# Optimization experiments

Hardware: AMD Instinct MI355X
Metric: run time of the kernel (lower is better)

Reference implementation:

```python
import jax, jax.numpy as jnp
import numpy as np

E, H, BLOCK = 1024, 64, 2048

def setup_inputs() -> dict:
    key = jax.random.key(0)
    kx, kk, kq, kv = jax.random.split(key, 4)
    s = 1.0 / np.sqrt(E)
    return {
        "x": jax.random.normal(kx, (16, 2048, E), dtype=jnp.float32),
        "Wk": jax.random.uniform(kk, (E, H), jnp.float32, -s, s),
        "Wq": jax.random.uniform(kq, (E, H), jnp.float32, -s, s),
        "Wv": jax.random.uniform(kv, (E, H), jnp.float32, -s, s),
    }

def reference(x, Wk, Wq, Wv):
    B, T, C = x.shape
    k = x @ Wk  # [B,T,H]
    q = x @ Wq
    v = x @ Wv
    scale = jnp.asarray(H, x.dtype) ** -0.5
    wei = jnp.einsum("bth,bsh->bts", q, k) * scale  # [B,T,T]
    causal = jnp.tril(jnp.ones((T, T), dtype=bool))
    wei = jnp.where(causal, wei, -jnp.inf)
    wei = jax.nn.softmax(wei, axis=-1)
    # dropout is identity in eval mode
    return jnp.einsum("bts,bsh->bth", wei, v)
```

## Files before the change

### kernel.cpp

```cpp
#include <hip/hip_runtime.h>


typedef __bf16 bf16x8 __attribute__((ext_vector_type(8)));
typedef float f32x4 __attribute__((ext_vector_type(4)));

constexpr int kE = 1024;
constexpr int kH = 64;
constexpr int kT = 2048;
constexpr int kB = 16;
constexpr int kM = kB * kT;
constexpr float kQScale = 0.125f * 1.44269504088896340736f;

#define MFMA16(a, b, c) __builtin_amdgcn_mfma_f32_16x16x32_bf16((a), (b), (c), 0, 0, 0)

__global__ __launch_bounds__(256)
void prep_w(const float* __restrict__ Wq, const float* __restrict__ Wk,
            const float* __restrict__ Wv, __bf16* __restrict__ WbT)
{
    __shared__ float tl[64][65];
    const int mat = blockIdx.x >> 4;
    const int k0 = (blockIdx.x & 15) * 64;
    const float* src = (mat == 0) ? Wq : (mat == 1) ? Wk : Wv;

    const int t = threadIdx.x;
    const int kr = t >> 2;
    const int cg = (t & 3) * 16;
    #pragma unroll
    for (int i = 0; i < 4; ++i) {
        float4 v = *(const float4*)&src[(size_t)(k0 + kr) * kH + cg + 4 * i];
        tl[cg + 4 * i + 0][kr] = v.x;
        tl[cg + 4 * i + 1][kr] = v.y;
        tl[cg + 4 * i + 2][kr] = v.z;
        tl[cg + 4 * i + 3][kr] = v.w;
    }
    __syncthreads();
    const int nl = t >> 2;
    const int kg = (t & 3) * 16;
    bf16x8 o0, o1;
    #pragma unroll
    for (int j = 0; j < 8; ++j) {
        o0[j] = (__bf16)tl[nl][kg + j];
        o1[j] = (__bf16)tl[nl][kg + 8 + j];
    }
    *(bf16x8*)&WbT[(size_t)(mat * 64 + nl) * kE + k0 + kg] = o0;
    *(bf16x8*)&WbT[(size_t)(mat * 64 + nl) * kE + k0 + kg + 8] = o1;
}

__global__ __launch_bounds__(256)
void qkv(const float* __restrict__ x, const __bf16* __restrict__ WbT,
         __bf16* __restrict__ qo, __bf16* __restrict__ ko, __bf16* __restrict__ vo)
{
    __shared__ __align__(16) __bf16 As[64][72];
    __shared__ __align__(16) __bf16 Bs[192][72];

    const int t = threadIdx.x;
    const int lane = t & 63;
    const int w = t >> 6;
    const int l15 = lane & 15;
    const int q = lane >> 4;
    const int row0 = blockIdx.x * 64;

    f32x4 acc[4][3];
    #pragma unroll
    for (int mt = 0; mt < 4; ++mt)
        #pragma unroll
        for (int nt = 0; nt < 3; ++nt) acc[mt][nt] = (f32x4){0.f, 0.f, 0.f, 0.f};

    const int sm = t >> 2;
    const int sc = (t & 3) * 16;

    for (int k0 = 0; k0 < kE; k0 += 64) {
        {
            float4 v0 = *(const float4*)&x[(size_t)(row0 + sm) * kE + k0 + sc];
            float4 v1 = *(const float4*)&x[(size_t)(row0 + sm) * kE + k0 + sc + 4];
            float4 v2 = *(const float4*)&x[(size_t)(row0 + sm) * kE + k0 + sc + 8];
            float4 v3 = *(const float4*)&x[(size_t)(row0 + sm) * kE + k0 + sc + 12];
            bf16x8 b0, b1;
            b0[0] = (__bf16)v0.x; b0[1] = (__bf16)v0.y; b0[2] = (__bf16)v0.z; b0[3] = (__bf16)v0.w;
            b0[4] = (__bf16)v1.x; b0[5] = (__bf16)v1.y; b0[6] = (__bf16)v1.z; b0[7] = (__bf16)v1.w;
            b1[0] = (__bf16)v2.x; b1[1] = (__bf16)v2.y; b1[2] = (__bf16)v2.z; b1[3] = (__bf16)v2.w;
            b1[4] = (__bf16)v3.x; b1[5] = (__bf16)v3.y; b1[6] = (__bf16)v3.z; b1[7] = (__bf16)v3.w;
            *(bf16x8*)&As[sm][sc] = b0;
            *(bf16x8*)&As[sm][sc + 8] = b1;
        }
        #pragma unroll
        for (int j = 0; j < 6; ++j) {
            int id = t + 256 * j;
            int n = id >> 3;
            int kc = (id & 7) * 8;
            *(bf16x8*)&Bs[n][kc] = *(const bf16x8*)&WbT[(size_t)n * kE + k0 + kc];
        }
        __syncthreads();

        #pragma unroll
        for (int ks = 0; ks < 2; ++ks) {
            bf16x8 a4[4];
            #pragma unroll
            for (int mt = 0; mt < 4; ++mt)
                a4[mt] = *(const bf16x8*)&As[mt * 16 + l15][ks * 32 + q * 8];
            #pragma unroll
            for (int nt = 0; nt < 3; ++nt) {
                bf16x8 b = *(const bf16x8*)&Bs[w * 48 + nt * 16 + l15][ks * 32 + q * 8];
                #pragma unroll
                for (int mt = 0; mt < 4; ++mt)
                    acc[mt][nt] = MFMA16(a4[mt], b, acc[mt][nt]);
            }
        }
        __syncthreads();
    }

    #pragma unroll
    for (int nt = 0; nt < 3; ++nt) {
        const int col0 = w * 48 + nt * 16;
        const int mat = col0 >> 6;
        const int c = (col0 & 63) + l15;
        __bf16* dst = (mat == 0) ? qo : (mat == 1) ? ko : vo;
        const float sc_ = (mat == 0) ? kQScale : 1.0f;
        #pragma unroll
        for (int mt = 0; mt < 4; ++mt)
            #pragma unroll
            for (int r = 0; r < 4; ++r) {
                const size_t row = row0 + mt * 16 + q * 4 + r;
                dst[row * kH + c] = (__bf16)(acc[mt][nt][r] * sc_);
            }
    }
}

__global__ __launch_bounds__(256)
void attn(const __bf16* __restrict__ qm, const __bf16* __restrict__ km,
          const __bf16* __restrict__ vm, float* __restrict__ out)
{
    __shared__ __align__(16) __bf16 Qs[64][72];
    __shared__ __align__(16) __bf16 Ks[64][72];
    __shared__ __align__(16) __bf16 Vt[64][72];
    __shared__ __align__(16) __bf16 Ps[4][16][72];

    const int t = threadIdx.x;
    const int lane = t & 63;
    const int w = t >> 6;
    const int l15 = lane & 15;
    const int q = lane >> 4;

    const int batch = blockIdx.x & 15;
    const int qi = 31 - (blockIdx.x >> 4);
    const int q0 = qi * 64;

    const __bf16* qb = qm + (size_t)batch * kT * kH;
    const __bf16* kb = km + (size_t)batch * kT * kH;
    const __bf16* vb = vm + (size_t)batch * kT * kH;

    const int sm = t >> 2;
    const int sc = (t & 3) * 16;

    *(bf16x8*)&Qs[sm][sc]     = *(const bf16x8*)&qb[(size_t)(q0 + sm) * kH + sc];
    *(bf16x8*)&Qs[sm][sc + 8] = *(const bf16x8*)&qb[(size_t)(q0 + sm) * kH + sc + 8];
    bf16x8 aq[2];
    #pragma unroll
    for (int ks = 0; ks < 2; ++ks)
        aq[ks] = *(const bf16x8*)&Qs[w * 16 + l15][ks * 32 + q * 8];

    f32x4 O[4];
    float m4[4], l4[4];
    #pragma unroll
    for (int i = 0; i < 4; ++i) {
        O[i] = (f32x4){0.f, 0.f, 0.f, 0.f};
        m4[i] = -1e30f; l4[i] = 0.f;
    }

    for (int kt = 0; kt <= qi; ++kt) {
        const int s0 = kt * 64;
        *(bf16x8*)&Ks[sm][sc]     = *(const bf16x8*)&kb[(size_t)(s0 + sm) * kH + sc];
        *(bf16x8*)&Ks[sm][sc + 8] = *(const bf16x8*)&kb[(size_t)(s0 + sm) * kH + sc + 8];
        {
            bf16x8 v0 = *(const bf16x8*)&vb[(size_t)(s0 + sm) * kH + sc];
            bf16x8 v1 = *(const bf16x8*)&vb[(size_t)(s0 + sm) * kH + sc + 8];
            #pragma unroll
            for (int j = 0; j < 8; ++j) {
                Vt[sc + j][sm] = v0[j];
                Vt[sc + 8 + j][sm] = v1[j];
            }
        }
        __syncthreads();

        f32x4 sacc[4];
        #pragma unroll
        for (int nt = 0; nt < 4; ++nt) sacc[nt] = (f32x4){0.f, 0.f, 0.f, 0.f};
        #pragma unroll
        for (int ks = 0; ks < 2; ++ks)
            #pragma unroll
            for (int nt = 0; nt < 4; ++nt) {
                bf16x8 b = *(const bf16x8*)&Ks[nt * 16 + l15][ks * 32 + q * 8];
                sacc[nt] = MFMA16(aq[ks], b, sacc[nt]);
            }

        if (kt == qi) {
            #pragma unroll
            for (int nt = 0; nt < 4; ++nt) {
                const int scol = s0 + nt * 16 + l15;
                #pragma unroll
                for (int r = 0; r < 4; ++r)
                    if (scol > q0 + w * 16 + q * 4 + r) sacc[nt][r] = -1e30f;
            }
        }

        #pragma unroll
        for (int r = 0; r < 4; ++r) {
            float mx = fmaxf(fmaxf(sacc[0][r], sacc[1][r]), fmaxf(sacc[2][r], sacc[3][r]));
            #pragma unroll
            for (int off = 1; off < 16; off <<= 1)
                mx = fmaxf(mx, __shfl_xor(mx, off, 16));
            const float mnew = fmaxf(m4[r], mx);
            const float alpha = __builtin_amdgcn_exp2f(m4[r] - mnew);
            float rs = 0.f;
            #pragma unroll
            for (int nt = 0; nt < 4; ++nt) {
                const float p = __builtin_amdgcn_exp2f(sacc[nt][r] - mnew);
                sacc[nt][r] = p;
                rs += p;
            }
            #pragma unroll
            for (int off = 1; off < 16; off <<= 1)
                rs += __shfl_xor(rs, off, 16);
            l4[r] = l4[r] * alpha + rs;
            m4[r] = mnew;
            #pragma unroll
            for (int ht = 0; ht < 4; ++ht) O[ht][r] *= alpha;
            #pragma unroll
            for (int nt = 0; nt < 4; ++nt)
                Ps[w][q * 4 + r][nt * 16 + l15] = (__bf16)sacc[nt][r];
        }

        #pragma unroll
        for (int ss = 0; ss < 2; ++ss) {
            bf16x8 ap = *(const bf16x8*)&Ps[w][l15][ss * 32 + q * 8];
            #pragma unroll
            for (int ht = 0; ht < 4; ++ht) {
                bf16x8 bv = *(const bf16x8*)&Vt[ht * 16 + l15][ss * 32 + q * 8];
                O[ht] = MFMA16(ap, bv, O[ht]);
            }
        }
        __syncthreads();
    }

    #pragma unroll
    for (int r = 0; r < 4; ++r) {
        const float inv = 1.0f / l4[r];
        const size_t row = (size_t)batch * kT + q0 + w * 16 + q * 4 + r;
        #pragma unroll
        for (int ht = 0; ht < 4; ++ht)
            out[row * kH + ht * 16 + l15] = O[ht][r] * inv;
    }
}

extern "C" void kernel_launch(void* const* d_in, const int* in_sizes, int n_in,
                              void* d_out, int out_size, void* d_ws, size_t ws_size,
                              hipStream_t stream)
{
    (void)in_sizes; (void)n_in; (void)out_size; (void)ws_size;
    const float* x  = (const float*)d_in[0];
    const float* Wk = (const float*)d_in[1];
    const float* Wq = (const float*)d_in[2];
    const float* Wv = (const float*)d_in[3];

    __bf16* WbT = (__bf16*)d_ws;
    __bf16* qb = WbT + (size_t)192 * kE;
    __bf16* kbuf = qb + (size_t)kM * kH;
    __bf16* vbuf = kbuf + (size_t)kM * kH;

    prep_w<<<48, 256, 0, stream>>>(Wq, Wk, Wv, WbT);
    qkv<<<kM / 64, 256, 0, stream>>>(x, WbT, qb, kbuf, vbuf);
    attn<<<kB * (kT / 64), 256, 0, stream>>>(qb, kbuf, vbuf, (float*)d_out);
}
```

Measured before the change: 271.6 us.

## Write V transposed in projection and restructure attention to single-wave register-fed blocks

The projection kernel now writes V transposed per batch ([B,H,T]) so the attention kernel can load V fragments straight from global memory without an LDS transpose. Attention is recast as one 64-thread wave per 16-query tile, with the MFMA operands swapped so S is computed transposed. K fragments are double-buffered in registers and prefetched from global, which removes the shared K/V tiles and block-wide barriers. The cost is more global/L2 traffic, since K/V tiles are no longer shared across four waves, plus a grid four times larger with smaller blocks.

```diff
diff --git a/kernel.cpp b/kernel.cpp
--- a/kernel.cpp
+++ b/kernel.cpp
@@ -2,6 +2,7 @@
 
 
 typedef __bf16 bf16x8 __attribute__((ext_vector_type(8)));
+typedef __bf16 bf16x4 __attribute__((ext_vector_type(4)));
 typedef float f32x4 __attribute__((ext_vector_type(4)));
 
 constexpr int kE = 1024;
@@ -48,7 +49,7 @@
 
 __global__ __launch_bounds__(256)
 void qkv(const float* __restrict__ x, const __bf16* __restrict__ WbT,
-         __bf16* __restrict__ qo, __bf16* __restrict__ ko, __bf16* __restrict__ vo)
+         __bf16* __restrict__ qo, __bf16* __restrict__ ko, __bf16* __restrict__ vT)
 {
     __shared__ __align__(16) __bf16 As[64][72];
     __shared__ __align__(16) __bf16 Bs[192][72];
@@ -109,78 +110,88 @@
         __syncthreads();
     }
 
+    const int batch = row0 >> 11;
+    const int tr0 = row0 & 2047;
     #pragma unroll
     for (int nt = 0; nt < 3; ++nt) {
         const int col0 = w * 48 + nt * 16;
         const int mat = col0 >> 6;
         const int c = (col0 & 63) + l15;
-        __bf16* dst = (mat == 0) ? qo : (mat == 1) ? ko : vo;
-        const float sc_ = (mat == 0) ? kQScale : 1.0f;
-        #pragma unroll
-        for (int mt = 0; mt < 4; ++mt)
-            #pragma unroll
-            for (int r = 0; r < 4; ++r) {
-                const size_t row = row0 + mt * 16 + q * 4 + r;
-                dst[row * kH + c] = (__bf16)(acc[mt][nt][r] * sc_);
+        if (mat == 2) {
+            #pragma unroll
+            for (int mt = 0; mt < 4; ++mt) {
+                const int trow = tr0 + mt * 16 + q * 4;
+                bf16x4 pk;
+                #pragma unroll
+                for (int r = 0; r < 4; ++r) pk[r] = (__bf16)acc[mt][nt][r];
+                *(bf16x4*)&vT[((size_t)batch * kH + c) * kT + trow] = pk;
             }
-    }
-}
-
-__global__ __launch_bounds__(256)
+        } else {
+            __bf16* dst = (mat == 0) ? qo : ko;
+            const float sc_ = (mat == 0) ? kQScale : 1.0f;
+            #pragma unroll
+            for (int mt = 0; mt < 4; ++mt)
+                #pragma unroll
+                for (int r = 0; r < 4; ++r) {
+                    const size_t row = row0 + mt * 16 + q * 4 + r;
+                    dst[row * kH + c] = (__bf16)(acc[mt][nt][r] * sc_);
+                }
+        }
+    }
+}
+
+__device__ __forceinline__ void load_kfrag(bf16x8 kf[8], const __bf16* kb,
+                                           int s0, int l15, int Q)
+{
+    #pragma unroll
+    for (int ks = 0; ks < 2; ++ks)
+        #pragma unroll
+        for (int nt = 0; nt < 4; ++nt)
+            kf[ks * 4 + nt] =
+                *(const bf16x8*)&kb[(size_t)(s0 + nt * 16 + l15) * kH + ks * 32 + Q * 8];
+}
+
+__global__ __launch_bounds__(64)
 void attn(const __bf16* __restrict__ qm, const __bf16* __restrict__ km,
-          const __bf16* __restrict__ vm, float* __restrict__ out)
-{
-    __shared__ __align__(16) __bf16 Qs[64][72];
-    __shared__ __align__(16) __bf16 Ks[64][72];
-    __shared__ __align__(16) __bf16 Vt[64][72];
-    __shared__ __align__(16) __bf16 Ps[4][16][72];
-
-    const int t = threadIdx.x;
-    const int lane = t & 63;
-    const int w = t >> 6;
+          const __bf16* __restrict__ vT, float* __restrict__ out)
+{
+    __shared__ __align__(16) __bf16 Ps[16][72];
+
+    const int lane = threadIdx.x;
     const int l15 = lane & 15;
-    const int q = lane >> 4;
+    const int Q = lane >> 4;
 
     const int batch = blockIdx.x & 15;
-    const int qi = 31 - (blockIdx.x >> 4);
-    const int q0 = qi * 64;
+    const int q16 = 127 - (blockIdx.x >> 4);
+    const int qrow = q16 * 16 + l15;
+    const int last = q16 >> 2;
 
     const __bf16* qb = qm + (size_t)batch * kT * kH;
     const __bf16* kb = km + (size_t)batch * kT * kH;
-    const __bf16* vb = vm + (size_t)batch * kT * kH;
-
-    const int sm = t >> 2;
-    const int sc = (t & 3) * 16;
-
-    *(bf16x8*)&Qs[sm][sc]     = *(const bf16x8*)&qb[(size_t)(q0 + sm) * kH + sc];
-    *(bf16x8*)&Qs[sm][sc + 8] = *(const bf16x8*)&qb[(size_t)(q0 + sm) * kH + sc + 8];
+    const __bf16* vb = vT + (size_t)batch * kH * kT;
+
     bf16x8 aq[2];
-    #pragma unroll
-    for (int ks = 0; ks < 2; ++ks)
-        aq[ks] = *(const bf16x8*)&Qs[w * 16 + l15][ks * 32 + q * 8];
+    aq[0] = *(const bf16x8*)&qb[(size_t)qrow * kH + Q * 8];
+    aq[1] = *(const bf16x8*)&qb[(size_t)qrow * kH + 32 + Q * 8];
 
     f32x4 O[4];
-    float m4[4], l4[4];
-    #pragma unroll
-    for (int i = 0; i < 4; ++i) {
-        O[i] = (f32x4){0.f, 0.f, 0.f, 0.f};
-        m4[i] = -1e30f; l4[i] = 0.f;
-    }
-
-    for (int kt = 0; kt <= qi; ++kt) {
+    #pragma unroll
+    for (int i = 0; i < 4; ++i) O[i] = (f32x4){0.f, 0.f, 0.f, 0.f};
+    float m_ = -3.0e38f, l_ = 0.f;
+
+    bf16x8 kfa[8], kfb[8];
+    load_kfrag(kfa, kb, 0, l15, Q);
+
+    auto step = [&](bf16x8 (&kcur)[8], bf16x8 (&knxt)[8], int kt) {
         const int s0 = kt * 64;
-        *(bf16x8*)&Ks[sm][sc]     = *(const bf16x8*)&kb[(size_t)(s0 + sm) * kH + sc];
-        *(bf16x8*)&Ks[sm][sc + 8] = *(const bf16x8*)&kb[(size_t)(s0 + sm) * kH + sc + 8];
-        {
-            bf16x8 v0 = *(const bf16x8*)&vb[(size_t)(s0 + sm) * kH + sc];
-            bf16x8 v1 = *(const bf16x8*)&vb[(size_t)(s0 + sm) * kH + sc + 8];
-            #pragma unroll
-            for (int j = 0; j < 8; ++j) {
-                Vt[sc + j][sm] = v0[j];
-                Vt[sc + 8 + j][sm] = v1[j];
-            }
-        }
-        __syncthreads();
+        bf16x8 vf[8];
+        #pragma unroll
+        for (int ht = 0; ht < 4; ++ht)
+            #pragma unroll
+            for (int ss = 0; ss < 2; ++ss)
+                vf[ht * 2 + ss] =
+                    *(const bf16x8*)&vb[(size_t)(ht * 16 + l15) * kT + s0 + ss * 32 + Q * 8];
+        if (kt < last) load_kfrag(knxt, kb, s0 + 64, l15, Q);
 
         f32x4 sacc[4];
         #pragma unroll
@@ -188,67 +199,72 @@
         #pragma unroll
         for (int ks = 0; ks < 2; ++ks)
             #pragma unroll
-            for (int nt = 0; nt < 4; ++nt) {
-                bf16x8 b = *(const bf16x8*)&Ks[nt * 16 + l15][ks * 32 + q * 8];
-                sacc[nt] = MFMA16(aq[ks], b, sacc[nt]);
-            }
-
-        if (kt == qi) {
-            #pragma unroll
-            for (int nt = 0; nt < 4; ++nt) {
-                const int scol = s0 + nt * 16 + l15;
+            for (int nt = 0; nt < 4; ++nt)
+                sacc[nt] = MFMA16(kcur[ks * 4 + nt], aq[ks], sacc[nt]);
+
+        if (kt == last) {
+            #pragma unroll
+            for (int nt = 0; nt < 4; ++nt)
                 #pragma unroll
                 for (int r = 0; r < 4; ++r)
-                    if (scol > q0 + w * 16 + q * 4 + r) sacc[nt][r] = -1e30f;
-            }
-        }
-
-        #pragma unroll
-        for (int r = 0; r < 4; ++r) {
-            float mx = fmaxf(fmaxf(sacc[0][r], sacc[1][r]), fmaxf(sacc[2][r], sacc[3][r]));
-            #pragma unroll
-            for (int off = 1; off < 16; off <<= 1)
-                mx = fmaxf(mx, __shfl_xor(mx, off, 16));
-            const float mnew = fmaxf(m4[r], mx);
-            const float alpha = __builtin_amdgcn_exp2f(m4[r] - mnew);
-            float rs = 0.f;
-            #pragma unroll
-            for (int nt = 0; nt < 4; ++nt) {
+                    if (s0 + nt * 16 + Q * 4 + r > qrow) sacc[nt][r] = -3.0e38f;
+        }
+
+        float mx = sacc[0][0];
+        #pragma unroll
+        for (int nt = 0; nt < 4; ++nt)
+            #pragma unroll
+            for (int r = 0; r < 4; ++r) mx = fmaxf(mx, sacc[nt][r]);
+        mx = fmaxf(mx, __shfl_xor(mx, 16));
+        mx = fmaxf(mx, __shfl_xor(mx, 32));
+        const float mnew = fmaxf(m_, mx);
+        const float alpha = __builtin_amdgcn_exp2f(m_ - mnew);
+        float rs = 0.f;
+        #pragma unroll
+        for (int nt = 0; nt < 4; ++nt)
+            #pragma unroll
+            for (int r = 0; r < 4; ++r) {
                 const float p = __builtin_amdgcn_exp2f(sacc[nt][r] - mnew);
                 sacc[nt][r] = p;
                 rs += p;
             }
-            #pragma unroll
-            for (int off = 1; off < 16; off <<= 1)
-                rs += __shfl_xor(rs, off, 16);
-            l4[r] = l4[r] * alpha + rs;
-            m4[r] = mnew;
-            #pragma unroll
-            for (int ht = 0; ht < 4; ++ht) O[ht][r] *= alpha;
-            #pragma unroll
-            for (int nt = 0; nt < 4; ++nt)
-                Ps[w][q * 4 + r][nt * 16 + l15] = (__bf16)sacc[nt][r];
-        }
-
-        #pragma unroll
-        for (int ss = 0; ss < 2; ++ss) {
-            bf16x8 ap = *(const bf16x8*)&Ps[w][l15][ss * 32 + q * 8];
-            #pragma unroll
-            for (int ht = 0; ht < 4; ++ht) {
-                bf16x8 bv = *(const bf16x8*)&Vt[ht * 16 + l15][ss * 32 + q * 8];
-                O[ht] = MFMA16(ap, bv, O[ht]);
-            }
-        }
-        __syncthreads();
-    }
-
-    #pragma unroll
-    for (int r = 0; r < 4; ++r) {
-        const float inv = 1.0f / l4[r];
-        const size_t row = (size_t)batch * kT + q0 + w * 16 + q * 4 + r;
-        #pragma unroll
-        for (int ht = 0; ht < 4; ++ht)
-            out[row * kH + ht * 16 + l15] = O[ht][r] * inv;
+        rs += __shfl_xor(rs, 16);
+        rs += __shfl_xor(rs, 32);
+        l_ = l_ * alpha + rs;
+        m_ = mnew;
+        #pragma unroll
+        for (int ht = 0; ht < 4; ++ht) O[ht] *= alpha;
+
+        #pragma unroll
+        for (int nt = 0; nt < 4; ++nt) {
+            bf16x4 pk;
+            #pragma unroll
+            for (int r = 0; r < 4; ++r) pk[r] = (__bf16)sacc[nt][r];
+            *(bf16x4*)&Ps[l15][nt * 16 + Q * 4] = pk;
+        }
+        bf16x8 pb0 = *(const bf16x8*)&Ps[l15][Q * 8];
+        bf16x8 pb1 = *(const bf16x8*)&Ps[l15][32 + Q * 8];
+
+        #pragma unroll
+        for (int ht = 0; ht < 4; ++ht) {
+            O[ht] = MFMA16(vf[ht * 2 + 0], pb0, O[ht]);
+            O[ht] = MFMA16(vf[ht * 2 + 1], pb1, O[ht]);
+        }
+    };
+
+    for (int kt = 0; kt <= last; kt += 2) {
+        step(kfa, kfb, kt);
+        if (kt + 1 <= last) step(kfb, kfa, kt + 1);
+    }
+
+    const float inv = 1.0f / l_;
+    float* orow = out + ((size_t)batch * kT + qrow) * kH;
+    #pragma unroll
+    for (int ht = 0; ht < 4; ++ht) {
+        float4 o4;
+        o4.x = O[ht][0] * inv; o4.y = O[ht][1] * inv;
+        o4.z = O[ht][2] * inv; o4.w = O[ht][3] * inv;
+        *(float4*)&orow[ht * 16 + Q * 4] = o4;
     }
 }
 
@@ -263,11 +279,11 @@
     const float* Wv = (const float*)d_in[3];
 
     __bf16* WbT = (__bf16*)d_ws;
-    __bf16* qb = WbT + (size_t)192 * kE;
+    __bf16* qb  = WbT + (size_t)192 * kE;
     __bf16* kbuf = qb + (size_t)kM * kH;
-    __bf16* vbuf = kbuf + (size_t)kM * kH;
+    __bf16* vT   = kbuf + (size_t)kM * kH;
 
     prep_w<<<48, 256, 0, stream>>>(Wq, Wk, Wv, WbT);
-    qkv<<<kM / 64, 256, 0, stream>>>(x, WbT, qb, kbuf, vbuf);
-    attn<<<kB * (kT / 64), 256, 0, stream>>>(qb, kbuf, vbuf, (float*)d_out);
-}
+    qkv<<<kM / 64, 256, 0, stream>>>(x, WbT, qb, kbuf, vT);
+    attn<<<kB * 128, 64, 0, stream>>>(qb, kbuf, vT, (float*)d_out);
+}
```

Result: no change. 272.2 us (+0.2%).
